# Optimization experiments

Measured on AMD Instinct MI355X. Metric: run time of the kernel, lower is better.

The kernel has to match this reference:

```python
import jax, jax.numpy as jnp
import numpy as np

NUM_CAPS = 2          # NUM_CLASSES
R = 16 * 10 * 10 * 10 # num_route_nodes = 16000
NUM_ITERS = 3


def conv3d(x, w, b, stride):
    y = jax.lax.conv_general_dilated(
        x, w, window_strides=(stride, stride, stride), padding='VALID',
        dimension_numbers=('NCDHW', 'OIDHW', 'NCDHW'))
    return y + b[None, :, None, None, None]


def squash(t, axis=-1):
    n = jnp.linalg.norm(t, axis=axis, keepdims=True)
    scale = n ** 2 / (1 + n ** 2) / (n + 1e-8)
    return scale * t


def setup_inputs() -> dict:
    key = jax.random.key(0)
    ks = jax.random.split(key, 16)
    inp = {
        'x': jax.random.normal(ks[0], (16, 1, 29, 29, 29), jnp.float32),
        'conv1_w': 0.05 * jax.random.normal(ks[1], (128, 1, 3, 3, 3), jnp.float32),
        'conv1_b': jnp.zeros((128,), jnp.float32),
        # 8 primary capsules, each Conv3d(128,16,k=9,s=2), stacked cap-major
        'pcaps_w': 0.01 * jax.random.normal(ks[2], (8 * 16, 128, 9, 9, 9), jnp.float32),
        'pcaps_b': jnp.zeros((8 * 16,), jnp.float32),
        'route_w': 0.01 * jax.random.normal(ks[3], (NUM_CAPS, R, 8, 16), jnp.float32),
        'dec_w1': 0.05 * jax.random.normal(ks[4], (32, 512), jnp.float32),
        'dec_b1': jnp.zeros((512,), jnp.float32),
        'dec_w2': 0.05 * jax.random.normal(ks[5], (512, 2048), jnp.float32),
        'dec_b2': jnp.zeros((2048,), jnp.float32),
        'dec_w3': 0.02 * jax.random.normal(ks[6], (2048, 10240), jnp.float32),
        'dec_b3': jnp.zeros((10240,), jnp.float32),
        'dec_w4': 0.02 * jax.random.normal(ks[7], (10240, 27000), jnp.float32),
        'dec_b4': jnp.zeros((27000,), jnp.float32),
    }
    return inp


def reference(x, conv1_w, conv1_b, pcaps_w, pcaps_b, route_w,
              dec_w1, dec_b1, dec_w2, dec_b2, dec_w3, dec_b3, dec_w4, dec_b4):
    B = x.shape[0]
    # stem conv + relu: [B,128,27,27,27]
    h = jax.nn.relu(conv3d(x, conv1_w, conv1_b, 1))
    # primary capsules (8 convs fused into one): [B,128,10,10,10]
    p = conv3d(h, pcaps_w, pcaps_b, 2)
    # torch: per-capsule view(B,-1,1) then cat dim=-1 -> [B,16000,8]
    p = p.reshape(B, 8, R).transpose(0, 2, 1)
    u = squash(p, axis=-1)  # [B,R,8]

    # priors: x[:,None,:,None,:] @ W[None] -> [B,C,R,16] (singleton dim dropped)
    priors = jnp.einsum('bri,crio->bcro', u, route_w)
    priors_d = jax.lax.stop_gradient(priors)
    # torch logits have trailing dim 16 but are constant along it (delta is
    # broadcast), so [B,C,R,1] is mathematically identical.
    logits = jnp.zeros((B, NUM_CAPS, R, 1), priors.dtype)

    for i in range(NUM_ITERS):
        probs = jax.nn.softmax(logits, axis=1)  # over capsule axis
        if i == NUM_ITERS - 1:
            v = squash((probs * priors).sum(axis=2, keepdims=True))
        else:
            v = squash((probs * priors_d).sum(axis=2, keepdims=True))
            logits = logits + (priors_d * v).sum(axis=-1, keepdims=True)

    caps = v[:, :, 0, :]  # [B,C,16] (squeeze)
    classes = jnp.linalg.norm(caps, axis=-1)  # [B,C]

    # y=None branch: one-hot of argmax
    y = jax.nn.one_hot(jnp.argmax(classes, axis=1), NUM_CAPS, dtype=caps.dtype)
    d = (caps * y[:, :, None]).reshape(B, -1)  # [B,32]
    d = jax.nn.relu(d @ dec_w1 + dec_b1)
    d = jax.nn.relu(d @ dec_w2 + dec_b2)
    d = jax.nn.relu(d @ dec_w3 + dec_b3)
    recon = jax.nn.sigmoid(d @ dec_w4 + dec_b4)  # [B,27000]
    return classes, recon
```

## Files before the change

kernel.cpp:

```cpp
#include <hip/hip_runtime.h>
#include <hip/hip_bf16.h>

#define NB   16
#define C1   128
#define XS   29
#define HS   27
#define HSP  19683
#define PS   10
#define PSP  1000
#define RR   16000
#define NCAP 2
#define KTAP 729
#define HTOT 40310784L
#define SPTOT 314928

#define OFF_WT   0UL
#define OFF_H    11943936UL
#define OFF_SP   52254720UL
#define OFF_U    54302720UL
#define OFF_PRI  56350720UL
#define OFF_LOG  64542720UL
#define OFF_V    65055232UL
#define OFF_D0   65055744UL
#define OFF_D1   65056256UL
#define OFF_D2   65064448UL
#define OFF_D3   65097216UL
#define OFF_D4   65261056UL
#define OFF_PP   65693056UL
#define OFF_D3P  82077056UL
#define OFF_D4P  84698496UL

typedef __attribute__((ext_vector_type(8))) short bf16x8;
typedef __attribute__((ext_vector_type(4))) float f32x4;

#define GL2LDS16(g, l) __builtin_amdgcn_global_load_lds( \
    (const __attribute__((address_space(1))) void*)(g), \
    (__attribute__((address_space(3))) void*)(l), 16, 0, 0)

__global__ void prep_w2(const float* __restrict__ w, __hip_bfloat16* __restrict__ w2) {
    __shared__ float tile[32][33];
    int tap0 = blockIdx.x * 32;
    int ic0  = blockIdx.y * 32;
    int oc   = blockIdx.z;
    int tx = threadIdx.x & 31, ty = threadIdx.x >> 5;
    #pragma unroll
    for (int j = 0; j < 32; j += 8) {
        int tap = tap0 + tx, ic = ic0 + ty + j;
        if (tap < KTAP) tile[ty + j][tx] = w[(size_t)oc * 93312 + (size_t)ic * KTAP + tap];
    }
    __syncthreads();
    #pragma unroll
    for (int j = 0; j < 32; j += 8) {
        int tap = tap0 + ty + j, ic = ic0 + tx;
        if (tap < KTAP)
            w2[((size_t)tap * 128 + oc) * 128 + ic] = __float2bfloat16(tile[tx][ty + j]);
    }
}

__global__ __launch_bounds__(256) void conv1_relu(const float* __restrict__ x,
                                                  const float* __restrict__ w,
                                                  const float* __restrict__ bias,
                                                  __hip_bfloat16* __restrict__ h) {
    int t = threadIdx.x;
    int c = t & 127;
    float wr[27];
    #pragma unroll
    for (int k = 0; k < 27; k++) wr[k] = w[c * 27 + k];
    float bv = bias[c];
    int sp_base = blockIdx.x * 32 + (t >> 7);
    #pragma unroll 4
    for (int i = 0; i < 16; i++) {
        int spg = sp_base + i * 2;
        if (spg >= SPTOT) return;
        int b = spg / HSP, sp = spg % HSP;
        int z = sp / 729, y = (sp / 27) % 27, xx = sp % 27;
        const float* xb = x + (size_t)b * (XS * XS * XS) + ((size_t)z * XS + y) * XS + xx;
        float xv[27];
        #pragma unroll
        for (int dz = 0; dz < 3; dz++)
            #pragma unroll
            for (int dy = 0; dy < 3; dy++)
                #pragma unroll
                for (int dx = 0; dx < 3; dx++)
                    xv[(dz * 3 + dy) * 3 + dx] = xb[((size_t)dz * XS + dy) * XS + dx];
        float acc = bv;
        #pragma unroll
        for (int k = 0; k < 27; k++) acc = fmaf(xv[k], wr[k], acc);
        h[(size_t)spg * 128 + c] = __float2bfloat16(fmaxf(acc, 0.f));
    }
}

__global__ __launch_bounds__(512, 2) void pcaps_mfma(const ushort* __restrict__ hu,
                                                     const ushort* __restrict__ wu,
                                                     float* __restrict__ pp) {
    __shared__ __align__(16) ushort As[2 * 256 * 32];
    __shared__ __align__(16) ushort Bs[2 * 128 * 32];
    int t = threadIdx.x;
    int bid = blockIdx.x;
    int g = bid & 7;
    int m0 = (bid >> 3) * 256;
    int tap_begin = g * 92;
    int tap_end   = min(KTAP, tap_begin + 92);
    int KP = (tap_end - tap_begin) * 4;

    int a_base[2], a_seg[2];
    #pragma unroll
    for (int q = 0; q < 2; q++) {
        int idx = q * 512 + t;
        int row = idx >> 2;
        int m = m0 + row; if (m > 15999) m = 15999;
        int b = m / PSP, sp = m % PSP;
        int oz = sp / 100, oy = (sp / 10) % 10, ox = sp % 10;
        a_base[q] = (((b * HS + 2 * oz) * HS + 2 * oy) * HS + 2 * ox) * 128;
        a_seg[q]  = (((idx & 3) ^ ((idx >> 3) & 3))) * 8;
    }
    int b_base = (t >> 2) * 128;
    int b_seg  = (((t & 3) ^ ((t >> 3) & 3))) * 8;

    int lane = t & 63, wave = t >> 6;
    int wr = wave >> 1, wc = wave & 1;
    int l15 = lane & 15, kq = lane >> 4;
    int slot8 = (kq ^ ((l15 >> 1) & 3)) * 8;

    f32x4 acc[4][4];
    #pragma unroll
    for (int i = 0; i < 4; i++)
        #pragma unroll
        for (int j = 0; j < 4; j++) acc[i][j] = (f32x4)0.f;

#define STAGE(KPI, NB_)  {                                                   \
        int tap_ = tap_begin + ((KPI) >> 2), ich_ = ((KPI) & 3) * 32;        \
        int dz_ = tap_ / 81, dy_ = (tap_ / 9) % 9, dx_ = tap_ % 9;           \
        int toff_ = ((dz_ * HS + dy_) * HS + dx_) * 128 + ich_;              \
        const ushort* wt_ = wu + ((size_t)tap_ << 14) + ich_;                \
        ushort* ad_ = As + (NB_) * (256 * 32);                               \
        ushort* bd_ = Bs + (NB_) * (128 * 32);                               \
        GL2LDS16(hu + a_base[0] + toff_ + a_seg[0], ad_ + (size_t)t * 8);    \
        GL2LDS16(hu + a_base[1] + toff_ + a_seg[1], ad_ + (size_t)(512 + t) * 8); \
        GL2LDS16(wt_ + b_base + b_seg, bd_ + (size_t)t * 8);                 \
    }

    STAGE(0, 0);
    int cur = 0;
    for (int kp = 0; kp < KP; ++kp) {
        int nk = (kp + 1 < KP) ? kp + 1 : kp;
        STAGE(nk, cur ^ 1);
        asm volatile("s_waitcnt vmcnt(3)" ::: "memory");
        __builtin_amdgcn_s_barrier();
        const ushort* Ac = As + cur * (256 * 32);
        const ushort* Bc = Bs + cur * (128 * 32);
        bf16x8 av[4], bv[4];
        #pragma unroll
        for (int i = 0; i < 4; i++)
            av[i] = *(const bf16x8*)&Ac[(wr * 64 + i * 16 + l15) * 32 + slot8];
        #pragma unroll
        for (int j = 0; j < 4; j++)
            bv[j] = *(const bf16x8*)&Bc[(wc * 64 + j * 16 + l15) * 32 + slot8];
        #pragma unroll
        for (int i = 0; i < 4; i++)
            #pragma unroll
            for (int j = 0; j < 4; j++)
                acc[i][j] = __builtin_amdgcn_mfma_f32_16x16x32_bf16(av[i], bv[j], acc[i][j], 0, 0, 0);
        __builtin_amdgcn_s_barrier();
        cur ^= 1;
    }
#undef STAGE

    float* pg = pp + (size_t)g * 16000 * 128;
    #pragma unroll
    for (int i = 0; i < 4; i++) {
        int mbase = m0 + wr * 64 + i * 16 + kq * 4;
        #pragma unroll
        for (int j = 0; j < 4; j++) {
            int n = wc * 64 + j * 16 + l15;
            #pragma unroll
            for (int r = 0; r < 4; r++) {
                int m = mbase + r;
                if (m < 16000) pg[(size_t)m * 128 + n] = acc[i][j][r];
            }
        }
    }
}

__global__ void squash_red(const float* __restrict__ pp, const float* __restrict__ pb,
                           float* __restrict__ u) {
    __shared__ float rowv[2][128];
    int t = threadIdx.x;
    int m = blockIdx.x * 2 + (t >> 7);
    int ch = t & 127;
    float v = pb[ch];
    #pragma unroll
    for (int g = 0; g < 8; g++) v += pp[(size_t)g * 2048000 + (size_t)m * 128 + ch];
    rowv[t >> 7][ch] = v;
    __syncthreads();
    if (t < 32) {
        int row = t >> 4, rq = t & 15;
        int mm = blockIdx.x * 2 + row;
        int b = mm / PSP, s = mm % PSP;
        float vals[8], ss = 0.f;
        #pragma unroll
        for (int i = 0; i < 8; i++) { float x = rowv[row][i * 16 + rq]; vals[i] = x; ss += x * x; }
        float n = sqrtf(ss);
        float sc = ss / (1.f + ss) / (n + 1e-8f);
        float* dst = u + ((size_t)b * RR + rq * 1000 + s) * 8;
        #pragma unroll
        for (int i = 0; i < 8; i++) dst[i] = vals[i] * sc;
    }
}

__global__ void priors_k(const float* __restrict__ u, const float* __restrict__ rw,
                         float* __restrict__ pri) {
    __shared__ float wl[16][132];
    int bx = blockIdx.x; int c = bx / 1000; int r0 = (bx % 1000) * 16;
    int t = threadIdx.x;
    const float4* src = (const float4*)(rw + ((size_t)c * RR + r0) * 128);
    #pragma unroll
    for (int q = 0; q < 8; q++) {
        int idx = q * 256 + t;
        int row = idx >> 5, c4 = idx & 31;
        *(float4*)&wl[row][c4 * 4] = src[idx];
    }
    __syncthreads();
    int bb = t >> 4, rl = t & 15;
    const float* up = u + ((size_t)bb * RR + r0 + rl) * 8;
    float4 u0 = *(const float4*)up, u1 = *(const float4*)(up + 4);
    float uu[8] = {u0.x, u0.y, u0.z, u0.w, u1.x, u1.y, u1.z, u1.w};
    float out[16];
    #pragma unroll
    for (int o = 0; o < 16; o++) out[o] = 0.f;
    #pragma unroll
    for (int i = 0; i < 8; i++)
        #pragma unroll
        for (int o = 0; o < 16; o++) out[o] += uu[i] * wl[rl][i * 16 + o];
    float* dst = pri + ((size_t)(bb * 2 + c) * RR + r0 + rl) * 16;
    #pragma unroll
    for (int q = 0; q < 4; q++)
        *(float4*)&dst[q * 4] = make_float4(out[q*4], out[q*4+1], out[q*4+2], out[q*4+3]);
}

__global__ void route_s0(const float* __restrict__ pri, float* __restrict__ spart) {
    int b = blockIdx.x, chunk = blockIdx.y;
    int t = threadIdx.x, o = t & 15, rl = t >> 4;
    float acc0 = 0.f, acc1 = 0.f;
    for (int j = 0; j < 40; j++) {
        int r = chunk * 640 + j * 16 + rl;
        acc0 += pri[((size_t)(b * 2 + 0) * RR + r) * 16 + o];
        acc1 += pri[((size_t)(b * 2 + 1) * RR + r) * 16 + o];
    }
    __shared__ float red[2][16][17];
    red[0][rl][o] = acc0; red[1][rl][o] = acc1;
    __syncthreads();
    for (int step = 8; step >= 1; step >>= 1) {
        if (rl < step) {
            red[0][rl][o] += red[0][rl + step][o];
            red[1][rl][o] += red[1][rl + step][o];
        }
        __syncthreads();
    }
    if (rl == 0) {
        spart[((b * 25 + chunk) * 2 + 0) * 16 + o] = 0.5f * red[0][0][o];
        spart[((b * 25 + chunk) * 2 + 1) * 16 + o] = 0.5f * red[1][0][o];
    }
}

template<int MODE>
__global__ void route_iter(const float* __restrict__ pri, const float* __restrict__ v,
                           float* __restrict__ lg, float* __restrict__ spart) {
    int b = blockIdx.x, chunk = blockIdx.y;
    int t = threadIdx.x, o = t & 15, rl = t >> 4;
    float v0 = v[(b * 2 + 0) * 16 + o], v1 = v[(b * 2 + 1) * 16 + o];
    float acc0 = 0.f, acc1 = 0.f;
    for (int j = 0; j < 40; j++) {
        int r = chunk * 640 + j * 16 + rl;
        float p0 = pri[((size_t)(b * 2 + 0) * RR + r) * 16 + o];
        float p1 = pri[((size_t)(b * 2 + 1) * RR + r) * 16 + o];
        float d0 = p0 * v0, d1 = p1 * v1;
        #pragma unroll
        for (int w = 1; w < 16; w <<= 1) { d0 += __shfl_xor(d0, w); d1 += __shfl_xor(d1, w); }
        float l0, l1;
        if (MODE == 1) {
            l0 = d0; l1 = d1;
            if (o == 0) lg[(size_t)(b * 2 + 0) * RR + r] = d0;
            if (o == 1) lg[(size_t)(b * 2 + 1) * RR + r] = d1;
        } else {
            l0 = lg[(size_t)(b * 2 + 0) * RR + r] + d0;
            l1 = lg[(size_t)(b * 2 + 1) * RR + r] + d1;
        }
        float mx = fmaxf(l0, l1);
        float e0 = __expf(l0 - mx), e1 = __expf(l1 - mx);
        float inv = 1.f / (e0 + e1);
        acc0 += (e0 * inv) * p0;
        acc1 += (e1 * inv) * p1;
    }
    __shared__ float red[2][16][17];
    red[0][rl][o] = acc0; red[1][rl][o] = acc1;
    __syncthreads();
    for (int step = 8; step >= 1; step >>= 1) {
        if (rl < step) {
            red[0][rl][o] += red[0][rl + step][o];
            red[1][rl][o] += red[1][rl + step][o];
        }
        __syncthreads();
    }
    if (rl == 0) {
        spart[((b * 25 + chunk) * 2 + 0) * 16 + o] = red[0][0][o];
        spart[((b * 25 + chunk) * 2 + 1) * 16 + o] = red[1][0][o];
    }
}

__global__ void squash_v_parts(const float* __restrict__ spart, float* __restrict__ v) {
    int t = threadIdx.x;
    int bc = t >> 4, o = t & 15;
    int b = bc >> 1, c = bc & 1;
    float x = 0.f;
    for (int ch = 0; ch < 25; ch++) x += spart[((b * 25 + ch) * 2 + c) * 16 + o];
    __shared__ float sv[32][17];
    sv[bc][o] = x;
    __syncthreads();
    float ss = 0.f;
    #pragma unroll
    for (int i = 0; i < 16; i++) { float y = sv[bc][i]; ss += y * y; }
    float n = sqrtf(ss);
    float sc = ss / (1.f + ss) / (n + 1e-8f);
    v[bc * 16 + o] = x * sc;
}

__global__ void squash_v_cls(const float* __restrict__ spart, float* __restrict__ out,
                             float* __restrict__ d0) {
    int t = threadIdx.x;
    int bc = t >> 4, o = t & 15;
    int b = bc >> 1, c = bc & 1;
    float x = 0.f;
    for (int ch = 0; ch < 25; ch++) x += spart[((b * 25 + ch) * 2 + c) * 16 + o];
    __shared__ float sv[32][17];
    __shared__ float vv[32][17];
    __shared__ float cls[32];
    sv[bc][o] = x;
    __syncthreads();
    float ss = 0.f;
    #pragma unroll
    for (int i = 0; i < 16; i++) { float y = sv[bc][i]; ss += y * y; }
    float n = sqrtf(ss);
    float sc = ss / (1.f + ss) / (n + 1e-8f);
    vv[bc][o] = x * sc;
    __syncthreads();
    if (t < 32) {
        float s2 = 0.f;
        #pragma unroll
        for (int i = 0; i < 16; i++) { float y = vv[t][i]; s2 += y * y; }
        float nn = sqrtf(s2);
        cls[t] = nn; out[t] = nn;
    }
    __syncthreads();
    int bb = t >> 5, k = t & 31, cc = k >> 4;
    int win = (cls[bb * 2 + 1] > cls[bb * 2 + 0]) ? 1 : 0;
    d0[t] = (cc == win) ? vv[bb * 2 + cc][k & 15] : 0.f;
}

template<int K>
__global__ void dec_small(const float* __restrict__ din, const float* __restrict__ W,
                          const float* __restrict__ bias, float* __restrict__ dout, int N) {
    __shared__ float dl[16 * K];
    int t = threadIdx.x;
    for (int i = t; i < 16 * K; i += 256) dl[i] = din[i];
    __syncthreads();
    int n = blockIdx.x * 256 + t;
    if (n >= N) return;
    float acc[16];
    float bv = bias[n];
    #pragma unroll
    for (int b = 0; b < 16; b++) acc[b] = bv;
    for (int k = 0; k < K; k++) {
        float w = W[(size_t)k * N + n];
        #pragma unroll
        for (int b = 0; b < 16; b++) acc[b] += dl[b * K + k] * w;
    }
    #pragma unroll
    for (int b = 0; b < 16; b++) dout[(size_t)b * N + n] = fmaxf(acc[b], 0.f);
}

__global__ void dec_split(const float* __restrict__ din, const float* __restrict__ W,
                          float* __restrict__ part, int N, int K, int KC) {
    extern __shared__ float dl[];
    int t = threadIdx.x;
    int ky = blockIdx.y;
    int k0 = ky * KC;
    for (int i = t; i < 16 * KC; i += 256) {
        int b = i / KC, kk = i % KC;
        dl[i] = din[(size_t)b * K + k0 + kk];
    }
    __syncthreads();
    int n = blockIdx.x * 1024 + t * 4;
    if (n >= N) return;
    float4 acc[16];
    #pragma unroll
    for (int b = 0; b < 16; b++) acc[b] = make_float4(0.f, 0.f, 0.f, 0.f);
    const float* Wp = W + (size_t)k0 * N + n;
    for (int kk = 0; kk < KC; kk++) {
        float4 w = *(const float4*)&Wp[(size_t)kk * N];
        #pragma unroll
        for (int b = 0; b < 16; b++) {
            float dv = dl[b * KC + kk];
            acc[b].x += dv * w.x; acc[b].y += dv * w.y;
            acc[b].z += dv * w.z; acc[b].w += dv * w.w;
        }
    }
    #pragma unroll
    for (int b = 0; b < 16; b++)
        *(float4*)&part[((size_t)(ky * 16 + b)) * N + n] = acc[b];
}

__global__ void bias_act_sum(const float* __restrict__ part, const float* __restrict__ bias,
                             float* __restrict__ out, int N, int total, int sigm) {
    int gid = blockIdx.x * 256 + threadIdx.x;
    if (gid >= total) return;
    int b = gid / N, n = gid % N;
    float x = bias[n];
    #pragma unroll
    for (int ky = 0; ky < 16; ky++)
        x += part[((size_t)(ky * 16 + b)) * N + n];
    out[gid] = sigm ? (1.f / (1.f + __expf(-x))) : fmaxf(x, 0.f);
}

extern "C" void kernel_launch(void* const* d_in, const int* in_sizes, int n_in,
                              void* d_out, int out_size, void* d_ws, size_t ws_size,
                              hipStream_t stream) {
    const float* x        = (const float*)d_in[0];
    const float* conv1_w  = (const float*)d_in[1];
    const float* conv1_b  = (const float*)d_in[2];
    const float* pcaps_w  = (const float*)d_in[3];
    const float* pcaps_b  = (const float*)d_in[4];
    const float* route_w  = (const float*)d_in[5];
    const float* dec_w1   = (const float*)d_in[6];
    const float* dec_b1   = (const float*)d_in[7];
    const float* dec_w2   = (const float*)d_in[8];
    const float* dec_b2   = (const float*)d_in[9];
    const float* dec_w3   = (const float*)d_in[10];
    const float* dec_b3   = (const float*)d_in[11];
    const float* dec_w4   = (const float*)d_in[12];
    const float* dec_b4   = (const float*)d_in[13];
    float* out = (float*)d_out;

    float* ws = (float*)d_ws;
    __hip_bfloat16* w2 = (__hip_bfloat16*)(ws + OFF_WT);
    __hip_bfloat16* h  = (__hip_bfloat16*)(ws + OFF_H);
    float* spart = ws + OFF_SP;
    float* u    = ws + OFF_U;
    float* pri  = ws + OFF_PRI;
    float* lg   = ws + OFF_LOG;
    float* v    = ws + OFF_V;
    float* d0   = ws + OFF_D0;
    float* d1   = ws + OFF_D1;
    float* d2   = ws + OFF_D2;
    float* d3   = ws + OFF_D3;
    float* pp   = ws + OFF_PP;
    float* d3p  = ws + OFF_D3P;
    float* d4p  = ws + OFF_D4P;

    prep_w2<<<dim3(23, 4, 128), 256, 0, stream>>>(pcaps_w, w2);
    conv1_relu<<<(SPTOT + 31) / 32, 256, 0, stream>>>(x, conv1_w, conv1_b, h);

    pcaps_mfma<<<504, 512, 0, stream>>>((const ushort*)h, (const ushort*)w2, pp);
    squash_red<<<8000, 256, 0, stream>>>(pp, pcaps_b, u);

    priors_k<<<2000, 256, 0, stream>>>(u, route_w, pri);

    route_s0<<<dim3(16, 25), 256, 0, stream>>>(pri, spart);
    squash_v_parts<<<1, 512, 0, stream>>>(spart, v);
    route_iter<1><<<dim3(16, 25), 256, 0, stream>>>(pri, v, lg, spart);
    squash_v_parts<<<1, 512, 0, stream>>>(spart, v);
    route_iter<2><<<dim3(16, 25), 256, 0, stream>>>(pri, v, lg, spart);
    squash_v_cls<<<1, 512, 0, stream>>>(spart, out, d0);

    dec_small<32><<<2, 256, 0, stream>>>(d0, dec_w1, dec_b1, d1, 512);
    dec_small<512><<<8, 256, 0, stream>>>(d1, dec_w2, dec_b2, d2, 2048);

    dec_split<<<dim3(10, 16), 256, 16 * 128 * sizeof(float), stream>>>(d2, dec_w3, d3p, 10240, 2048, 128);
    bias_act_sum<<<(16 * 10240 + 255) / 256, 256, 0, stream>>>(d3p, dec_b3, d3, 10240, 16 * 10240, 0);

    dec_split<<<dim3(27, 16), 256, 16 * 640 * sizeof(float), stream>>>(d3, dec_w4, d4p, 27000, 10240, 640);
    bias_act_sum<<<(16 * 27000 + 255) / 256, 256, 0, stream>>>(d4p, dec_b4, out + 32, 27000, 16 * 27000, 1);
}
```

Baseline: 1.226 ms.

## Restructure primary-capsule conv as LDS-resident input tiles with channel-group layout

Replaces the implicit-GEMM pcaps kernel, which staged im2col A tiles per tap through LDS double buffers, with a kernel that loads a whole 4-channel input slab for one batch and z-slice into LDS once. It then sweeps all taps from that slab with MFMAs, reusing the staged activations across the 81 dz/dy positions. The stem conv now writes a transposed channel-group layout padded to 28 in x, and the weights are repacked so each MFMA K-chunk pairs two dx taps with four input channels. The dx=8 remainder taps get special handling. The aim is less redundant global traffic for overlapping windows, at the cost of more complex indexing, wasted rows from padding 200 outputs to 13 fragments, and a full vmcnt(0) wait per phase with no prefetch overlap.

```diff
diff --git a/kernel.cpp b/kernel.cpp
--- a/kernel.cpp
+++ b/kernel.cpp
@@ -2,17 +2,19 @@
 #include <hip/hip_bf16.h>
 
 #define NB   16
-#define C1   128
 #define XS   29
 #define HS   27
 #define HSP  19683
-#define PS   10
 #define PSP  1000
 #define RR   16000
-#define NCAP 2
 #define KTAP 729
-#define HTOT 40310784L
 #define SPTOT 314928
+
+#define HT_SLOT   81648UL
+#define HT_TOTAL  41803776UL
+#define HT_PLANE  3024
+#define W2B_CH    4096
+#define W2B_ICG   376832UL
 
 #define OFF_WT   0UL
 #define OFF_H    11943936UL
@@ -25,7 +27,6 @@
 #define OFF_D1   65056256UL
 #define OFF_D2   65064448UL
 #define OFF_D3   65097216UL
-#define OFF_D4   65261056UL
 #define OFF_PP   65693056UL
 #define OFF_D3P  82077056UL
 #define OFF_D4P  84698496UL
@@ -37,147 +38,167 @@
     (const __attribute__((address_space(1))) void*)(g), \
     (__attribute__((address_space(3))) void*)(l), 16, 0, 0)
 
-__global__ void prep_w2(const float* __restrict__ w, __hip_bfloat16* __restrict__ w2) {
-    __shared__ float tile[32][33];
-    int tap0 = blockIdx.x * 32;
-    int ic0  = blockIdx.y * 32;
-    int oc   = blockIdx.z;
-    int tx = threadIdx.x & 31, ty = threadIdx.x >> 5;
-    #pragma unroll
-    for (int j = 0; j < 32; j += 8) {
-        int tap = tap0 + tx, ic = ic0 + ty + j;
-        if (tap < KTAP) tile[ty + j][tx] = w[(size_t)oc * 93312 + (size_t)ic * KTAP + tap];
-    }
-    __syncthreads();
-    #pragma unroll
-    for (int j = 0; j < 32; j += 8) {
-        int tap = tap0 + ty + j, ic = ic0 + tx;
-        if (tap < KTAP)
-            w2[((size_t)tap * 128 + oc) * 128 + ic] = __float2bfloat16(tile[tx][ty + j]);
-    }
-}
-
-__global__ __launch_bounds__(256) void conv1_relu(const float* __restrict__ x,
-                                                  const float* __restrict__ w,
-                                                  const float* __restrict__ bias,
-                                                  __hip_bfloat16* __restrict__ h) {
+__global__ void prep_w2b(const float* __restrict__ w, ushort* __restrict__ w2b) {
+    int gid = blockIdx.x * 256 + threadIdx.x;
+    int oc  = gid / 11776;
+    int r   = gid % 11776;
+    int icg = r / 368;
+    int r2  = r % 368;
+    int c = r2 >> 2, kq = r2 & 3;
+    const float* wb = w + (size_t)oc * 93312 + (size_t)icg * 4 * KTAP;
+    ushort vals[8];
+    #pragma unroll
+    for (int j = 0; j < 8; j++) {
+        int ic = j & 3, half = j >> 2;
+        float v = 0.f;
+        if (c < 81) {
+            int tap = c * 9 + 2 * kq + half;
+            v = wb[ic * KTAP + tap];
+        } else {
+            int dzy = (c - 81) * 8 + 2 * kq + half;
+            if (dzy <= 80) v = wb[ic * KTAP + dzy * 9 + 8];
+        }
+        __hip_bfloat16 hv = __float2bfloat16(v);
+        vals[j] = *(ushort*)&hv;
+    }
+    ushort* dst = w2b + ((size_t)((icg * 92 + c) * 4 + kq) * 128 + oc) * 8;
+    #pragma unroll
+    for (int j = 0; j < 8; j++) dst[j] = vals[j];
+}
+
+__global__ __launch_bounds__(256) void conv1_relu_t(const float* __restrict__ x,
+                                                    const float* __restrict__ w,
+                                                    const float* __restrict__ bias,
+                                                    ushort* __restrict__ hT) {
+    __shared__ ushort lt[32][132];
     int t = threadIdx.x;
     int c = t & 127;
     float wr[27];
     #pragma unroll
     for (int k = 0; k < 27; k++) wr[k] = w[c * 27 + k];
     float bv = bias[c];
-    int sp_base = blockIdx.x * 32 + (t >> 7);
+    int sp0 = blockIdx.x * 32;
     #pragma unroll 4
     for (int i = 0; i < 16; i++) {
-        int spg = sp_base + i * 2;
-        if (spg >= SPTOT) return;
-        int b = spg / HSP, sp = spg % HSP;
-        int z = sp / 729, y = (sp / 27) % 27, xx = sp % 27;
-        const float* xb = x + (size_t)b * (XS * XS * XS) + ((size_t)z * XS + y) * XS + xx;
-        float xv[27];
-        #pragma unroll
-        for (int dz = 0; dz < 3; dz++)
+        int spl = i * 2 + (t >> 7);
+        int spg = sp0 + spl;
+        if (spg < SPTOT) {
+            int b = spg / HSP, sp = spg % HSP;
+            int z = sp / 729, y = (sp / 27) % 27, xx = sp % 27;
+            const float* xb = x + (size_t)b * (XS * XS * XS) + ((size_t)z * XS + y) * XS + xx;
+            float xv[27];
             #pragma unroll
-            for (int dy = 0; dy < 3; dy++)
+            for (int dz = 0; dz < 3; dz++)
                 #pragma unroll
-                for (int dx = 0; dx < 3; dx++)
-                    xv[(dz * 3 + dy) * 3 + dx] = xb[((size_t)dz * XS + dy) * XS + dx];
-        float acc = bv;
-        #pragma unroll
-        for (int k = 0; k < 27; k++) acc = fmaf(xv[k], wr[k], acc);
-        h[(size_t)spg * 128 + c] = __float2bfloat16(fmaxf(acc, 0.f));
-    }
-}
-
-__global__ __launch_bounds__(512, 2) void pcaps_mfma(const ushort* __restrict__ hu,
-                                                     const ushort* __restrict__ wu,
+                for (int dy = 0; dy < 3; dy++)
+                    #pragma unroll
+                    for (int dx = 0; dx < 3; dx++)
+                        xv[(dz * 3 + dy) * 3 + dx] = xb[((size_t)dz * XS + dy) * XS + dx];
+            float acc = bv;
+            #pragma unroll
+            for (int k = 0; k < 27; k++) acc = fmaf(xv[k], wr[k], acc);
+            __hip_bfloat16 hv = __float2bfloat16(fmaxf(acc, 0.f));
+            lt[spl][c] = *(ushort*)&hv;
+        }
+    }
+    __syncthreads();
+    #pragma unroll
+    for (int q = 0; q < 4; q++) {
+        int gidx = q * 256 + t;
+        int icg = gidx >> 5, spl = gidx & 31;
+        int spg = sp0 + spl;
+        if (spg < SPTOT) {
+            int b = spg / HSP, sp = spg % HSP;
+            int z = sp / 729, y = (sp / 27) % 27, xx = sp % 27;
+            *(short4*)(hT + (size_t)(icg * 16 + b) * HT_SLOT
+                          + ((size_t)(z * 27 + y) * 28 + xx) * 4) =
+                *(const short4*)&lt[spl][icg * 4];
+        }
+    }
+}
+
+__global__ __launch_bounds__(512, 4) void pcaps_conv(const ushort* __restrict__ hT,
+                                                     const ushort* __restrict__ w2b,
                                                      float* __restrict__ pp) {
-    __shared__ __align__(16) ushort As[2 * 256 * 32];
-    __shared__ __align__(16) ushort Bs[2 * 128 * 32];
+    __shared__ __align__(16) ushort AT[36288];
     int t = threadIdx.x;
     int bid = blockIdx.x;
     int g = bid & 7;
-    int m0 = (bid >> 3) * 256;
-    int tap_begin = g * 92;
-    int tap_end   = min(KTAP, tap_begin + 92);
-    int KP = (tap_end - tap_begin) * 4;
-
-    int a_base[2], a_seg[2];
-    #pragma unroll
-    for (int q = 0; q < 2; q++) {
-        int idx = q * 512 + t;
-        int row = idx >> 2;
-        int m = m0 + row; if (m > 15999) m = 15999;
-        int b = m / PSP, sp = m % PSP;
-        int oz = sp / 100, oy = (sp / 10) % 10, ox = sp % 10;
-        a_base[q] = (((b * HS + 2 * oz) * HS + 2 * oy) * HS + 2 * ox) * 128;
-        a_seg[q]  = (((idx & 3) ^ ((idx >> 3) & 3))) * 8;
-    }
-    int b_base = (t >> 2) * 128;
-    int b_seg  = (((t & 3) ^ ((t >> 3) & 3))) * 8;
+    int rest = bid >> 3;
+    int b = rest / 5, ozt = rest % 5;
+    int z0 = ozt * 4;
 
     int lane = t & 63, wave = t >> 6;
-    int wr = wave >> 1, wc = wave & 1;
+    int ocb = wave * 16;
     int l15 = lane & 15, kq = lane >> 4;
-    int slot8 = (kq ^ ((l15 >> 1) & 3)) * 8;
-
-    f32x4 acc[4][4];
-    #pragma unroll
-    for (int i = 0; i < 4; i++)
-        #pragma unroll
-        for (int j = 0; j < 4; j++) acc[i][j] = (f32x4)0.f;
-
-#define STAGE(KPI, NB_)  {                                                   \
-        int tap_ = tap_begin + ((KPI) >> 2), ich_ = ((KPI) & 3) * 32;        \
-        int dz_ = tap_ / 81, dy_ = (tap_ / 9) % 9, dx_ = tap_ % 9;           \
-        int toff_ = ((dz_ * HS + dy_) * HS + dx_) * 128 + ich_;              \
-        const ushort* wt_ = wu + ((size_t)tap_ << 14) + ich_;                \
-        ushort* ad_ = As + (NB_) * (256 * 32);                               \
-        ushort* bd_ = Bs + (NB_) * (128 * 32);                               \
-        GL2LDS16(hu + a_base[0] + toff_ + a_seg[0], ad_ + (size_t)t * 8);    \
-        GL2LDS16(hu + a_base[1] + toff_ + a_seg[1], ad_ + (size_t)(512 + t) * 8); \
-        GL2LDS16(wt_ + b_base + b_seg, bd_ + (size_t)t * 8);                 \
-    }
-
-    STAGE(0, 0);
-    int cur = 0;
-    for (int kp = 0; kp < KP; ++kp) {
-        int nk = (kp + 1 < KP) ? kp + 1 : kp;
-        STAGE(nk, cur ^ 1);
-        asm volatile("s_waitcnt vmcnt(3)" ::: "memory");
-        __builtin_amdgcn_s_barrier();
-        const ushort* Ac = As + cur * (256 * 32);
-        const ushort* Bc = Bs + cur * (128 * 32);
-        bf16x8 av[4], bv[4];
-        #pragma unroll
-        for (int i = 0; i < 4; i++)
-            av[i] = *(const bf16x8*)&Ac[(wr * 64 + i * 16 + l15) * 32 + slot8];
-        #pragma unroll
-        for (int j = 0; j < 4; j++)
-            bv[j] = *(const bf16x8*)&Bc[(wc * 64 + j * 16 + l15) * 32 + slot8];
-        #pragma unroll
-        for (int i = 0; i < 4; i++)
+
+    int vox[13];
+    #pragma unroll
+    for (int f = 0; f < 13; f++) {
+        int lr = f * 16 + l15; if (lr > 199) lr = 199;
+        int ozl = lr / 100; int rem = lr % 100;
+        int oy = rem / 10, ox = rem % 10;
+        vox[f] = (2 * ozl) * 6048 + (2 * oy) * 224 + (2 * ox) * 8;
+    }
+
+    f32x4 acc[13];
+    #pragma unroll
+    for (int f = 0; f < 13; f++) acc[f] = (f32x4)0.f;
+
+    int bvoff = (kq * 128 + ocb + l15) * 8;
+
+    for (int ph = 0; ph < 4; ++ph) {
+        int icg = g * 4 + ph;
+        const ushort* src = hT + (size_t)(icg * 16 + b) * HT_SLOT + (size_t)z0 * HT_PLANE;
+        if (ph) __syncthreads();
+        #pragma unroll
+        for (int q = 0; q < 9; q++) {
+            int gi = q * 512 + t;
+            if (gi < 4536)
+                GL2LDS16(src + (size_t)gi * 8, AT + (size_t)gi * 8);
+        }
+        asm volatile("s_waitcnt vmcnt(0)" ::: "memory");
+        __syncthreads();
+
+        const ushort* wB = w2b + (size_t)icg * W2B_ICG;
+        bf16x8 bv = *(const bf16x8*)(wB + bvoff);
+        for (int c = 0; c < 81; ++c) {
+            bf16x8 bvn = *(const bf16x8*)(wB + (size_t)(c + 1) * W2B_CH + bvoff);
+            int coff = (c / 9) * 6048 + (c % 9) * 224 + kq * 16;
             #pragma unroll
-            for (int j = 0; j < 4; j++)
-                acc[i][j] = __builtin_amdgcn_mfma_f32_16x16x32_bf16(av[i], bv[j], acc[i][j], 0, 0, 0);
-        __builtin_amdgcn_s_barrier();
-        cur ^= 1;
-    }
-#undef STAGE
-
-    float* pg = pp + (size_t)g * 16000 * 128;
-    #pragma unroll
-    for (int i = 0; i < 4; i++) {
-        int mbase = m0 + wr * 64 + i * 16 + kq * 4;
-        #pragma unroll
-        for (int j = 0; j < 4; j++) {
-            int n = wc * 64 + j * 16 + l15;
+            for (int f = 0; f < 13; f++) {
+                bf16x8 av = *(const bf16x8*)((const char*)AT + vox[f] + coff);
+                acc[f] = __builtin_amdgcn_mfma_f32_16x16x32_bf16(av, bv, acc[f], 0, 0, 0);
+            }
+            bv = bvn;
+        }
+        for (int cc = 0; cc < 11; ++cc) {
+            int nxt = (cc == 10) ? 91 : 82 + cc;
+            bf16x8 bvn = *(const bf16x8*)(wB + (size_t)nxt * W2B_CH + bvoff);
+            int dzy0 = cc * 8 + 2 * kq;
+            int dzy1 = dzy0 + 1;
+            int o0 = (dzy0 / 9) * 6048 + (dzy0 % 9) * 224 + 64;
+            int o1 = (dzy1 / 9) * 6048 + (dzy1 % 9) * 224 + 64;
             #pragma unroll
-            for (int r = 0; r < 4; r++) {
-                int m = mbase + r;
-                if (m < 16000) pg[(size_t)m * 128 + n] = acc[i][j][r];
+            for (int f = 0; f < 13; f++) {
+                union { bf16x8 v; short4 h[2]; } a;
+                a.h[0] = *(const short4*)((const char*)AT + vox[f] + o0);
+                a.h[1] = *(const short4*)((const char*)AT + vox[f] + o1);
+                acc[f] = __builtin_amdgcn_mfma_f32_16x16x32_bf16(a.v, bv, acc[f], 0, 0, 0);
             }
+            bv = bvn;
+        }
+    }
+
+    float* pg = pp + (size_t)g * 2048000;
+    int mbase = b * 1000 + ozt * 200;
+    #pragma unroll
+    for (int f = 0; f < 13; f++) {
+        #pragma unroll
+        for (int r = 0; r < 4; r++) {
+            int lr = f * 16 + kq * 4 + r;
+            if (lr < 200)
+                pg[(size_t)(mbase + lr) * 128 + ocb + l15] = acc[f][r];
         }
     }
 }
@@ -442,8 +463,8 @@
     float* out = (float*)d_out;
 
     float* ws = (float*)d_ws;
-    __hip_bfloat16* w2 = (__hip_bfloat16*)(ws + OFF_WT);
-    __hip_bfloat16* h  = (__hip_bfloat16*)(ws + OFF_H);
+    ushort* w2b = (ushort*)(ws + OFF_WT);
+    ushort* hT  = (ushort*)(ws + OFF_H);
     float* spart = ws + OFF_SP;
     float* u    = ws + OFF_U;
     float* pri  = ws + OFF_PRI;
@@ -457,10 +478,11 @@
     float* d3p  = ws + OFF_D3P;
     float* d4p  = ws + OFF_D4P;
 
-    prep_w2<<<dim3(23, 4, 128), 256, 0, stream>>>(pcaps_w, w2);
-    conv1_relu<<<(SPTOT + 31) / 32, 256, 0, stream>>>(x, conv1_w, conv1_b, h);
-
-    pcaps_mfma<<<504, 512, 0, stream>>>((const ushort*)h, (const ushort*)w2, pp);
+    prep_w2b<<<5888, 256, 0, stream>>>(pcaps_w, w2b);
+    conv1_relu_t<<<9842, 256, 0, stream>>>(x, conv1_w, conv1_b, hT);
+    hipMemsetAsync(hT + HT_TOTAL, 0, 8192, stream);
+
+    pcaps_conv<<<640, 512, 0, stream>>>(hT, w2b, pp);
     squash_red<<<8000, 256, 0, stream>>>(pp, pcaps_b, u);
 
     priors_k<<<2000, 256, 0, stream>>>(u, route_w, pri);
```

Result: no change. 1.215 ms (-0.9%).
